# Kernel optimization log

Hardware: AMD Instinct MI355X
Metric: run time of the kernel (lower is better)

The kernel has to match this reference:

```python
import jax, jax.numpy as jnp
import numpy as np

S = 1                      # half window
K = 2 * S + 1              # box kernel size = 3
SZ = float(K ** 3)         # kernel volume = 27
EPS = 1e-5


def _box_sum(x, s=S):
    """3D box-sum filter with replicate (edge) padding.

    Equivalent to Conv3d(1,1,kernel=2s+1,padding=s,padding_mode='replicate')
    with an all-ones kernel, computed via separable sliding sums (cumsum
    difference) along D, H, W -- O(1) work per voxel per axis.
    x: [B, 1, D, H, W]
    """
    k = 2 * s + 1
    x = jnp.pad(x, ((0, 0), (0, 0), (s, s), (s, s), (s, s)), mode='edge')
    for ax in (2, 3, 4):
        c = jnp.cumsum(x, axis=ax)
        n = c.shape[ax]
        upper = jax.lax.slice_in_dim(c, k - 1, n, axis=ax)
        zero = jnp.zeros_like(jax.lax.slice_in_dim(c, 0, 1, axis=ax))
        lower = jnp.concatenate(
            [zero, jax.lax.slice_in_dim(c, 0, n - k, axis=ax)], axis=ax)
        x = upper - lower  # sliding window sum of width k
    return x


def setup_inputs() -> dict:
    key = jax.random.key(0)
    k1, k2 = jax.random.split(key)
    shape = (2, 1, 192, 192, 192)  # [B, C=1, D, H, W]
    return {
        "im_fixed": jax.random.normal(k1, shape, dtype=jnp.float32),
        "im_moving": jax.random.normal(k2, shape, dtype=jnp.float32),
    }


def reference(im_fixed, im_moving):
    u_F = _box_sum(im_fixed) / SZ          # local mean of fixed
    u_M = _box_sum(im_moving) / SZ         # local mean of moving
    dF = im_fixed - u_F
    dM = im_moving - u_M
    cross = _box_sum(dF * dM)
    var_F = _box_sum(dF * dF)
    var_M = _box_sum(dM * dM)
    z = cross * cross / (var_F * var_M + EPS)
    return -1.0 * jnp.mean(z, axis=(1, 2, 3, 4))  # [B]
```

## Files before the change

kernel.cpp:

```cpp
#include <hip/hip_runtime.h>

#define DIM 192
#define DD  (DIM * DIM)
#define DDD (DIM * DIM * DIM)
#define INV27 (1.0f / 27.0f)
#define EPS 1e-5f

#define TY 8
#define ZC 12
#define NRS (TY + 4)
#define NPR (TY + 2)

__device__ __forceinline__ int iclamp(int v, int hi) {
    return v < 0 ? 0 : (v > hi ? hi : v);
}

__global__ __launch_bounds__(512) void lcc_fused(
    const float* __restrict__ F, const float* __restrict__ M,
    float* __restrict__ out)
{
    __shared__ float RSf[NRS][DIM];
    __shared__ float RSm[NRS][DIM];
    __shared__ float PRS[3][NPR][DIM];
    __shared__ float wred[8];

    const int tid = threadIdx.x;
    const int w   = tid >> 6;
    const int t   = tid & 63;
    const int x   = 3 * t;

    const int y0 = blockIdx.y * TY;
    const int z0 = blockIdx.x * ZC;
    const int z1 = z0 + ZC;
    const int b  = blockIdx.z;

    const float* f = F + (size_t)b * DDD;
    const float* m = M + (size_t)b * DDD;

    const int  row1a = iclamp(y0 - 2 + w, DIM - 1);
    const bool has1b = (w < NRS - 8);
    const int  row1b = iclamp(y0 + 6 + w, DIM - 1);

    const int  tA    = w + 1;
    const int  prowA = iclamp(y0 - 1 + tA, DIM - 1);
    const bool hasB  = (w == 0) || (w == 7);
    const int  tB    = (w == 0) ? 0 : NPR - 1;
    const int  prowB = iclamp(y0 - 1 + tB, DIM - 1);

    const int sAm = iclamp(prowA - 1, DIM - 1) - y0 + 2;
    const int sAc = prowA - y0 + 2;
    const int sAp = iclamp(prowA + 1, DIM - 1) - y0 + 2;
    const int sBm = iclamp(prowB - 1, DIM - 1) - y0 + 2;
    const int sBc = prowB - y0 + 2;
    const int sBp = iclamp(prowB + 1, DIM - 1) - y0 + 2;

    const int yo  = y0 + w;
    const int tOm = iclamp(yo - 1, DIM - 1) - y0 + 1;
    const int tOc = w + 1;
    const int tOp = iclamp(yo + 1, DIM - 1) - y0 + 1;

    const int zpLo = (z0 - 1 > 0) ? z0 - 1 : 0;
    const int zpHi = (z1 < DIM - 1) ? z1 : DIM - 1;
    const int zcStart = (z0 - 2 > -1) ? z0 - 2 : -1;
    const int zcEnd   = z1 + 2;

    float rAf[3][3], rAm[3][3], rBf[3][3], rBm[3][3];
    float pmv[9], pcv[9], pnv[9];
#pragma unroll
    for (int i = 0; i < 3; ++i)
#pragma unroll
        for (int j = 0; j < 3; ++j) {
            rAf[i][j] = 0.f; rAm[i][j] = 0.f; rBf[i][j] = 0.f; rBm[i][j] = 0.f;
        }
#pragma unroll
    for (int i = 0; i < 9; ++i) { pmv[i] = 0.f; pcv[i] = 0.f; pnv[i] = 0.f; }

    float accz = 0.f;

    for (int zc = zcStart; zc <= zcEnd; ++zc) {
        const bool doLoad = (zc <= zpHi + 1);
        const int zcl = iclamp(zc, DIM - 1);
        const size_t zoff = (size_t)zcl * DD;

        float fa0 = 0, fa1 = 0, fa2 = 0, ma0 = 0, ma1 = 0, ma2 = 0;
        float fb0 = 0, fb1 = 0, fb2 = 0, mb0 = 0, mb1 = 0, mb2 = 0;
        if (doLoad) {
            const float* fr = f + zoff + (size_t)row1a * DIM + x;
            const float* mr = m + zoff + (size_t)row1a * DIM + x;
            fa0 = fr[0]; fa1 = fr[1]; fa2 = fr[2];
            ma0 = mr[0]; ma1 = mr[1]; ma2 = mr[2];
            if (has1b) {
                const float* fr2 = f + zoff + (size_t)row1b * DIM + x;
                const float* mr2 = m + zoff + (size_t)row1b * DIM + x;
                fb0 = fr2[0]; fb1 = fr2[1]; fb2 = fr2[2];
                mb0 = mr2[0]; mb1 = mr2[1]; mb2 = mr2[2];
            }
        }

        {
            const int zq = zc - 2;
            if (zq >= zpLo) {
#pragma unroll
                for (int i = 0; i < 9; ++i) { pmv[i] = pcv[i]; pcv[i] = pnv[i]; }
                if (zq <= zpHi) {
#pragma unroll
                    for (int q = 0; q < 3; ++q) {
                        float3 u0 = *(const float3*)&PRS[q][tOm][x];
                        float3 u1 = *(const float3*)&PRS[q][tOc][x];
                        float3 u2 = *(const float3*)&PRS[q][tOp][x];
                        pnv[q * 3 + 0] = u0.x + u1.x + u2.x;
                        pnv[q * 3 + 1] = u0.y + u1.y + u2.y;
                        pnv[q * 3 + 2] = u0.z + u1.z + u2.z;
                    }
                }
                const int zo = zc - 3;
                if (zo >= z0 && zo < z1) {
#pragma unroll
                    for (int j = 0; j < 3; ++j) {
                        float a0 = (zo == 0) ? pcv[j]     : pmv[j];
                        float a1 = (zo == 0) ? pcv[3 + j] : pmv[3 + j];
                        float a2 = (zo == 0) ? pcv[6 + j] : pmv[6 + j];
                        float c0 = (zo == DIM - 1) ? pcv[j]     : pnv[j];
                        float c1 = (zo == DIM - 1) ? pcv[3 + j] : pnv[3 + j];
                        float c2 = (zo == DIM - 1) ? pcv[6 + j] : pnv[6 + j];
                        float cross = a0 + pcv[j]     + c0;
                        float vF    = a1 + pcv[3 + j] + c1;
                        float vM    = a2 + pcv[6 + j] + c2;
                        accz += cross * cross / (vF * vM + EPS);
                    }
                }
            }
        }

        if (doLoad) {
            {
                float aL = __shfl(fa2, t - 1); aL = (t == 0)  ? fa0 : aL;
                float aR = __shfl(fa0, t + 1); aR = (t == 63) ? fa2 : aR;
                float cL = __shfl(ma2, t - 1); cL = (t == 0)  ? ma0 : cL;
                float cR = __shfl(ma0, t + 1); cR = (t == 63) ? ma2 : cR;
                *(float3*)&RSf[w][x] = make_float3(aL + fa0 + fa1, fa0 + fa1 + fa2, fa1 + fa2 + aR);
                *(float3*)&RSm[w][x] = make_float3(cL + ma0 + ma1, ma0 + ma1 + ma2, ma1 + ma2 + cR);
            }
            if (has1b) {
                float aL = __shfl(fb2, t - 1); aL = (t == 0)  ? fb0 : aL;
                float aR = __shfl(fb0, t + 1); aR = (t == 63) ? fb2 : aR;
                float cL = __shfl(mb2, t - 1); cL = (t == 0)  ? mb0 : cL;
                float cR = __shfl(mb0, t + 1); cR = (t == 63) ? mb2 : cR;
                *(float3*)&RSf[8 + w][x] = make_float3(aL + fb0 + fb1, fb0 + fb1 + fb2, fb1 + fb2 + aR);
                *(float3*)&RSm[8 + w][x] = make_float3(cL + mb0 + mb1, mb0 + mb1 + mb2, mb1 + mb2 + cR);
            }
        }
        __syncthreads();

        const int  zp    = zc - 1;
        const bool liveP = (zp >= zpLo) && (zp <= zpHi);

        float cfA0 = 0, cfA1 = 0, cfA2 = 0, cmA0 = 0, cmA1 = 0, cmA2 = 0;
        float cfB0 = 0, cfB1 = 0, cfB2 = 0, cmB0 = 0, cmB1 = 0, cmB2 = 0;
        if (liveP) {
            const size_t poff = (size_t)zp * DD;
            const float* fv = f + poff + (size_t)prowA * DIM + x;
            const float* mv = m + poff + (size_t)prowA * DIM + x;
            cfA0 = fv[0]; cfA1 = fv[1]; cfA2 = fv[2];
            cmA0 = mv[0]; cmA1 = mv[1]; cmA2 = mv[2];
            if (hasB) {
                const float* fv2 = f + poff + (size_t)prowB * DIM + x;
                const float* mv2 = m + poff + (size_t)prowB * DIM + x;
                cfB0 = fv2[0]; cfB1 = fv2[1]; cfB2 = fv2[2];
                cmB0 = mv2[0]; cmB1 = mv2[1]; cmB2 = mv2[2];
            }
        }

        if (doLoad) {
            {
                float3 q0 = *(const float3*)&RSf[sAm][x];
                float3 q1 = *(const float3*)&RSf[sAc][x];
                float3 q2 = *(const float3*)&RSf[sAp][x];
                float3 r0 = *(const float3*)&RSm[sAm][x];
                float3 r1 = *(const float3*)&RSm[sAc][x];
                float3 r2 = *(const float3*)&RSm[sAp][x];
#pragma unroll
                for (int j = 0; j < 3; ++j) {
                    rAf[0][j] = rAf[1][j]; rAf[1][j] = rAf[2][j];
                    rAm[0][j] = rAm[1][j]; rAm[1][j] = rAm[2][j];
                }
                rAf[2][0] = q0.x + q1.x + q2.x;
                rAf[2][1] = q0.y + q1.y + q2.y;
                rAf[2][2] = q0.z + q1.z + q2.z;
                rAm[2][0] = r0.x + r1.x + r2.x;
                rAm[2][1] = r0.y + r1.y + r2.y;
                rAm[2][2] = r0.z + r1.z + r2.z;
            }
            if (hasB) {
                float3 q0 = *(const float3*)&RSf[sBm][x];
                float3 q1 = *(const float3*)&RSf[sBc][x];
                float3 q2 = *(const float3*)&RSf[sBp][x];
                float3 r0 = *(const float3*)&RSm[sBm][x];
                float3 r1 = *(const float3*)&RSm[sBc][x];
                float3 r2 = *(const float3*)&RSm[sBp][x];
#pragma unroll
                for (int j = 0; j < 3; ++j) {
                    rBf[0][j] = rBf[1][j]; rBf[1][j] = rBf[2][j];
                    rBm[0][j] = rBm[1][j]; rBm[1][j] = rBm[2][j];
                }
                rBf[2][0] = q0.x + q1.x + q2.x;
                rBf[2][1] = q0.y + q1.y + q2.y;
                rBf[2][2] = q0.z + q1.z + q2.z;
                rBm[2][0] = r0.x + r1.x + r2.x;
                rBm[2][1] = r0.y + r1.y + r2.y;
                rBm[2][2] = r0.z + r1.z + r2.z;
            }
        }

        if (liveP) {
            {
                float uf0 = (rAf[0][0] + rAf[1][0] + rAf[2][0]) * INV27;
                float uf1 = (rAf[0][1] + rAf[1][1] + rAf[2][1]) * INV27;
                float uf2 = (rAf[0][2] + rAf[1][2] + rAf[2][2]) * INV27;
                float um0 = (rAm[0][0] + rAm[1][0] + rAm[2][0]) * INV27;
                float um1 = (rAm[0][1] + rAm[1][1] + rAm[2][1]) * INV27;
                float um2 = (rAm[0][2] + rAm[1][2] + rAm[2][2]) * INV27;
                float dF0 = cfA0 - uf0, dF1 = cfA1 - uf1, dF2 = cfA2 - uf2;
                float dM0 = cmA0 - um0, dM1 = cmA1 - um1, dM2 = cmA2 - um2;
                float qc0 = dF0 * dM0, qc1 = dF1 * dM1, qc2 = dF2 * dM2;
                float qf0 = dF0 * dF0, qf1 = dF1 * dF1, qf2 = dF2 * dF2;
                float qm0 = dM0 * dM0, qm1 = dM1 * dM1, qm2 = dM2 * dM2;
                float cL = __shfl(qc2, t - 1); cL = (t == 0)  ? qc0 : cL;
                float cR = __shfl(qc0, t + 1); cR = (t == 63) ? qc2 : cR;
                float fL = __shfl(qf2, t - 1); fL = (t == 0)  ? qf0 : fL;
                float fR = __shfl(qf0, t + 1); fR = (t == 63) ? qf2 : fR;
                float mL = __shfl(qm2, t - 1); mL = (t == 0)  ? qm0 : mL;
                float mR = __shfl(qm0, t + 1); mR = (t == 63) ? qm2 : mR;
                *(float3*)&PRS[0][tA][x] = make_float3(cL + qc0 + qc1, qc0 + qc1 + qc2, qc1 + qc2 + cR);
                *(float3*)&PRS[1][tA][x] = make_float3(fL + qf0 + qf1, qf0 + qf1 + qf2, qf1 + qf2 + fR);
                *(float3*)&PRS[2][tA][x] = make_float3(mL + qm0 + qm1, qm0 + qm1 + qm2, qm1 + qm2 + mR);
            }
            if (hasB) {
                float uf0 = (rBf[0][0] + rBf[1][0] + rBf[2][0]) * INV27;
                float uf1 = (rBf[0][1] + rBf[1][1] + rBf[2][1]) * INV27;
                float uf2 = (rBf[0][2] + rBf[1][2] + rBf[2][2]) * INV27;
                float um0 = (rBm[0][0] + rBm[1][0] + rBm[2][0]) * INV27;
                float um1 = (rBm[0][1] + rBm[1][1] + rBm[2][1]) * INV27;
                float um2 = (rBm[0][2] + rBm[1][2] + rBm[2][2]) * INV27;
                float dF0 = cfB0 - uf0, dF1 = cfB1 - uf1, dF2 = cfB2 - uf2;
                float dM0 = cmB0 - um0, dM1 = cmB1 - um1, dM2 = cmB2 - um2;
                float qc0 = dF0 * dM0, qc1 = dF1 * dM1, qc2 = dF2 * dM2;
                float qf0 = dF0 * dF0, qf1 = dF1 * dF1, qf2 = dF2 * dF2;
                float qm0 = dM0 * dM0, qm1 = dM1 * dM1, qm2 = dM2 * dM2;
                float cL = __shfl(qc2, t - 1); cL = (t == 0)  ? qc0 : cL;
                float cR = __shfl(qc0, t + 1); cR = (t == 63) ? qc2 : cR;
                float fL = __shfl(qf2, t - 1); fL = (t == 0)  ? qf0 : fL;
                float fR = __shfl(qf0, t + 1); fR = (t == 63) ? qf2 : fR;
                float mL = __shfl(qm2, t - 1); mL = (t == 0)  ? qm0 : mL;
                float mR = __shfl(qm0, t + 1); mR = (t == 63) ? qm2 : mR;
                *(float3*)&PRS[0][tB][x] = make_float3(cL + qc0 + qc1, qc0 + qc1 + qc2, qc1 + qc2 + cR);
                *(float3*)&PRS[1][tB][x] = make_float3(fL + qf0 + qf1, qf0 + qf1 + qf2, qf1 + qf2 + fR);
                *(float3*)&PRS[2][tB][x] = make_float3(mL + qm0 + qm1, qm0 + qm1 + qm2, qm1 + qm2 + mR);
            }
        }
        __syncthreads();
    }

    float s = accz;
#pragma unroll
    for (int off = 32; off > 0; off >>= 1) s += __shfl_down(s, off, 64);
    if (t == 0) wred[w] = s;
    __syncthreads();
    if (tid == 0) {
        float tot = 0.f;
#pragma unroll
        for (int i = 0; i < 8; ++i) tot += wred[i];
        atomicAdd(&out[b], tot * (-1.0f / (float)DDD));
    }
}

extern "C" void kernel_launch(void* const* d_in, const int* in_sizes, int n_in,
                              void* d_out, int out_size, void* d_ws, size_t ws_size,
                              hipStream_t stream)
{
    const float* F = (const float*)d_in[0];
    const float* M = (const float*)d_in[1];
    float* out = (float*)d_out;

    hipMemsetAsync(d_out, 0, (size_t)out_size * sizeof(float), stream);

    dim3 grid(DIM / ZC, DIM / TY, 2);
    lcc_fused<<<grid, 512, 0, stream>>>(F, M, out);
}
```

Baseline: 195.8 us.

## Grow y-tile to 12 rows and rebalance per-warp row assignment

Raises the y tile from 8 to 12 rows per block, so the 4-row halo recomputation is amortised over more output rows. The per-warp row assignments are rebalanced so that every warp loads two input rows, six warps compute a second product row, and four warps handle a second output row. It also hoists the centre-voxel global loads ahead of the first barrier and adds a launch-bounds minimum-blocks hint of 4. In exchange it raises register pressure from the duplicated z-ring buffers and adds LDS use per block, which may lower occupancy or cause spills.

```diff
diff --git a/kernel.cpp b/kernel.cpp
--- a/kernel.cpp
+++ b/kernel.cpp
@@ -6,16 +6,88 @@
 #define INV27 (1.0f / 27.0f)
 #define EPS 1e-5f
 
-#define TY 8
+#define TY 12
 #define ZC 12
 #define NRS (TY + 4)
 #define NPR (TY + 2)
 
+
 __device__ __forceinline__ int iclamp(int v, int hi) {
     return v < 0 ? 0 : (v > hi ? hi : v);
 }
 
-__global__ __launch_bounds__(512) void lcc_fused(
+__device__ __forceinline__ float3 xrowsum(float v0, float v1, float v2, int t) {
+    float L = __shfl(v2, t - 1); L = (t == 0)  ? v0 : L;
+    float R = __shfl(v0, t + 1); R = (t == 63) ? v2 : R;
+    return make_float3(L + v0 + v1, v0 + v1 + v2, v1 + v2 + R);
+}
+
+__device__ __forceinline__ void ringpush(float r[3][3], const float RS[][DIM],
+                                         int sm_, int sc_, int sp_, int x) {
+    float3 q0 = *(const float3*)&RS[sm_][x];
+    float3 q1 = *(const float3*)&RS[sc_][x];
+    float3 q2 = *(const float3*)&RS[sp_][x];
+    r[0][0] = r[1][0]; r[0][1] = r[1][1]; r[0][2] = r[1][2];
+    r[1][0] = r[2][0]; r[1][1] = r[2][1]; r[1][2] = r[2][2];
+    r[2][0] = q0.x + q1.x + q2.x;
+    r[2][1] = q0.y + q1.y + q2.y;
+    r[2][2] = q0.z + q1.z + q2.z;
+}
+
+__device__ __forceinline__ void products(const float rf[3][3], const float rm[3][3],
+                                         float cf0, float cf1, float cf2,
+                                         float cm0, float cm1, float cm2,
+                                         int t, int tt, int x,
+                                         float P[3][NPR][DIM]) {
+    float uf0 = (rf[0][0] + rf[1][0] + rf[2][0]) * INV27;
+    float uf1 = (rf[0][1] + rf[1][1] + rf[2][1]) * INV27;
+    float uf2 = (rf[0][2] + rf[1][2] + rf[2][2]) * INV27;
+    float um0 = (rm[0][0] + rm[1][0] + rm[2][0]) * INV27;
+    float um1 = (rm[0][1] + rm[1][1] + rm[2][1]) * INV27;
+    float um2 = (rm[0][2] + rm[1][2] + rm[2][2]) * INV27;
+    float dF0 = cf0 - uf0, dF1 = cf1 - uf1, dF2 = cf2 - uf2;
+    float dM0 = cm0 - um0, dM1 = cm1 - um1, dM2 = cm2 - um2;
+    float3 rc = xrowsum(dF0 * dM0, dF1 * dM1, dF2 * dM2, t);
+    float3 rq = xrowsum(dF0 * dF0, dF1 * dF1, dF2 * dF2, t);
+    float3 rr = xrowsum(dM0 * dM0, dM1 * dM1, dM2 * dM2, t);
+    *(float3*)&P[0][tt][x] = rc;
+    *(float3*)&P[1][tt][x] = rq;
+    *(float3*)&P[2][tt][x] = rr;
+}
+
+__device__ __forceinline__ void prs_read(const float P[3][NPR][DIM],
+                                         int tm, int tc, int tp, int x, float pn[9]) {
+#pragma unroll
+    for (int q = 0; q < 3; ++q) {
+        float3 u0 = *(const float3*)&P[q][tm][x];
+        float3 u1 = *(const float3*)&P[q][tc][x];
+        float3 u2 = *(const float3*)&P[q][tp][x];
+        pn[q * 3 + 0] = u0.x + u1.x + u2.x;
+        pn[q * 3 + 1] = u0.y + u1.y + u2.y;
+        pn[q * 3 + 2] = u0.z + u1.z + u2.z;
+    }
+}
+
+__device__ __forceinline__ float zwindow(const float pm[9], const float pc[9],
+                                         const float pn[9], int zo) {
+    float a = 0.f;
+#pragma unroll
+    for (int j = 0; j < 3; ++j) {
+        float a0 = (zo == 0) ? pc[j]     : pm[j];
+        float a1 = (zo == 0) ? pc[3 + j] : pm[3 + j];
+        float a2 = (zo == 0) ? pc[6 + j] : pm[6 + j];
+        float c0 = (zo == DIM - 1) ? pc[j]     : pn[j];
+        float c1 = (zo == DIM - 1) ? pc[3 + j] : pn[3 + j];
+        float c2 = (zo == DIM - 1) ? pc[6 + j] : pn[6 + j];
+        float cross = a0 + pc[j]     + c0;
+        float vF    = a1 + pc[3 + j] + c1;
+        float vM    = a2 + pc[6 + j] + c2;
+        a += cross * cross / (vF * vM + EPS);
+    }
+    return a;
+}
+
+__global__ __launch_bounds__(512, 4) void lcc_fused(
     const float* __restrict__ F, const float* __restrict__ M,
     float* __restrict__ out)
 {
@@ -37,14 +109,13 @@
     const float* f = F + (size_t)b * DDD;
     const float* m = M + (size_t)b * DDD;
 
-    const int  row1a = iclamp(y0 - 2 + w, DIM - 1);
-    const bool has1b = (w < NRS - 8);
-    const int  row1b = iclamp(y0 + 6 + w, DIM - 1);
+    const int row1a = iclamp(y0 - 2 + w, DIM - 1);
+    const int row1b = iclamp(y0 + 6 + w, DIM - 1);
 
     const int  tA    = w + 1;
     const int  prowA = iclamp(y0 - 1 + tA, DIM - 1);
-    const bool hasB  = (w == 0) || (w == 7);
-    const int  tB    = (w == 0) ? 0 : NPR - 1;
+    const bool hasB  = (w < 6);
+    const int  tB    = (w < 5) ? 9 + w : 0;
     const int  prowB = iclamp(y0 - 1 + tB, DIM - 1);
 
     const int sAm = iclamp(prowA - 1, DIM - 1) - y0 + 2;
@@ -54,10 +125,15 @@
     const int sBc = prowB - y0 + 2;
     const int sBp = iclamp(prowB + 1, DIM - 1) - y0 + 2;
 
-    const int yo  = y0 + w;
-    const int tOm = iclamp(yo - 1, DIM - 1) - y0 + 1;
-    const int tOc = w + 1;
-    const int tOp = iclamp(yo + 1, DIM - 1) - y0 + 1;
+    const int  yo1  = y0 + w;
+    const int  t1m  = iclamp(yo1 - 1, DIM - 1) - y0 + 1;
+    const int  t1c  = w + 1;
+    const int  t1p  = iclamp(yo1 + 1, DIM - 1) - y0 + 1;
+    const bool has2 = (w < 4);
+    const int  yo2  = y0 + 8 + w;
+    const int  t2m  = iclamp(yo2 - 1, DIM - 1) - y0 + 1;
+    const int  t2c  = 9 + w;
+    const int  t2p  = iclamp(yo2 + 1, DIM - 1) - y0 + 1;
 
     const int zpLo = (z0 - 1 > 0) ? z0 - 1 : 0;
     const int zpHi = (z1 < DIM - 1) ? z1 : DIM - 1;
@@ -65,7 +141,7 @@
     const int zcEnd   = z1 + 2;
 
     float rAf[3][3], rAm[3][3], rBf[3][3], rBm[3][3];
-    float pmv[9], pcv[9], pnv[9];
+    float pm1[9], pc1[9], pn1[9], pm2[9], pc2[9], pn2[9];
 #pragma unroll
     for (int i = 0; i < 3; ++i)
 #pragma unroll
@@ -73,14 +149,19 @@
             rAf[i][j] = 0.f; rAm[i][j] = 0.f; rBf[i][j] = 0.f; rBm[i][j] = 0.f;
         }
 #pragma unroll
-    for (int i = 0; i < 9; ++i) { pmv[i] = 0.f; pcv[i] = 0.f; pnv[i] = 0.f; }
+    for (int i = 0; i < 9; ++i) {
+        pm1[i] = 0.f; pc1[i] = 0.f; pn1[i] = 0.f;
+        pm2[i] = 0.f; pc2[i] = 0.f; pn2[i] = 0.f;
+    }
 
     float accz = 0.f;
 
     for (int zc = zcStart; zc <= zcEnd; ++zc) {
         const bool doLoad = (zc <= zpHi + 1);
-        const int zcl = iclamp(zc, DIM - 1);
+        const int  zcl  = iclamp(zc, DIM - 1);
         const size_t zoff = (size_t)zcl * DD;
+        const int  zp    = zc - 1;
+        const bool liveP = (zp >= zpLo) && (zp <= zpHi);
 
         float fa0 = 0, fa1 = 0, fa2 = 0, ma0 = 0, ma1 = 0, ma2 = 0;
         float fb0 = 0, fb1 = 0, fb2 = 0, mb0 = 0, mb1 = 0, mb2 = 0;
@@ -89,72 +170,11 @@
             const float* mr = m + zoff + (size_t)row1a * DIM + x;
             fa0 = fr[0]; fa1 = fr[1]; fa2 = fr[2];
             ma0 = mr[0]; ma1 = mr[1]; ma2 = mr[2];
-            if (has1b) {
-                const float* fr2 = f + zoff + (size_t)row1b * DIM + x;
-                const float* mr2 = m + zoff + (size_t)row1b * DIM + x;
-                fb0 = fr2[0]; fb1 = fr2[1]; fb2 = fr2[2];
-                mb0 = mr2[0]; mb1 = mr2[1]; mb2 = mr2[2];
-            }
-        }
-
-        {
-            const int zq = zc - 2;
-            if (zq >= zpLo) {
-#pragma unroll
-                for (int i = 0; i < 9; ++i) { pmv[i] = pcv[i]; pcv[i] = pnv[i]; }
-                if (zq <= zpHi) {
-#pragma unroll
-                    for (int q = 0; q < 3; ++q) {
-                        float3 u0 = *(const float3*)&PRS[q][tOm][x];
-                        float3 u1 = *(const float3*)&PRS[q][tOc][x];
-                        float3 u2 = *(const float3*)&PRS[q][tOp][x];
-                        pnv[q * 3 + 0] = u0.x + u1.x + u2.x;
-                        pnv[q * 3 + 1] = u0.y + u1.y + u2.y;
-                        pnv[q * 3 + 2] = u0.z + u1.z + u2.z;
-                    }
-                }
-                const int zo = zc - 3;
-                if (zo >= z0 && zo < z1) {
-#pragma unroll
-                    for (int j = 0; j < 3; ++j) {
-                        float a0 = (zo == 0) ? pcv[j]     : pmv[j];
-                        float a1 = (zo == 0) ? pcv[3 + j] : pmv[3 + j];
-                        float a2 = (zo == 0) ? pcv[6 + j] : pmv[6 + j];
-                        float c0 = (zo == DIM - 1) ? pcv[j]     : pnv[j];
-                        float c1 = (zo == DIM - 1) ? pcv[3 + j] : pnv[3 + j];
-                        float c2 = (zo == DIM - 1) ? pcv[6 + j] : pnv[6 + j];
-                        float cross = a0 + pcv[j]     + c0;
-                        float vF    = a1 + pcv[3 + j] + c1;
-                        float vM    = a2 + pcv[6 + j] + c2;
-                        accz += cross * cross / (vF * vM + EPS);
-                    }
-                }
-            }
-        }
-
-        if (doLoad) {
-            {
-                float aL = __shfl(fa2, t - 1); aL = (t == 0)  ? fa0 : aL;
-                float aR = __shfl(fa0, t + 1); aR = (t == 63) ? fa2 : aR;
-                float cL = __shfl(ma2, t - 1); cL = (t == 0)  ? ma0 : cL;
-                float cR = __shfl(ma0, t + 1); cR = (t == 63) ? ma2 : cR;
-                *(float3*)&RSf[w][x] = make_float3(aL + fa0 + fa1, fa0 + fa1 + fa2, fa1 + fa2 + aR);
-                *(float3*)&RSm[w][x] = make_float3(cL + ma0 + ma1, ma0 + ma1 + ma2, ma1 + ma2 + cR);
-            }
-            if (has1b) {
-                float aL = __shfl(fb2, t - 1); aL = (t == 0)  ? fb0 : aL;
-                float aR = __shfl(fb0, t + 1); aR = (t == 63) ? fb2 : aR;
-                float cL = __shfl(mb2, t - 1); cL = (t == 0)  ? mb0 : cL;
-                float cR = __shfl(mb0, t + 1); cR = (t == 63) ? mb2 : cR;
-                *(float3*)&RSf[8 + w][x] = make_float3(aL + fb0 + fb1, fb0 + fb1 + fb2, fb1 + fb2 + aR);
-                *(float3*)&RSm[8 + w][x] = make_float3(cL + mb0 + mb1, mb0 + mb1 + mb2, mb1 + mb2 + cR);
-            }
-        }
-        __syncthreads();
-
-        const int  zp    = zc - 1;
-        const bool liveP = (zp >= zpLo) && (zp <= zpHi);
-
+            const float* fr2 = f + zoff + (size_t)row1b * DIM + x;
+            const float* mr2 = m + zoff + (size_t)row1b * DIM + x;
+            fb0 = fr2[0]; fb1 = fr2[1]; fb2 = fr2[2];
+            mb0 = mr2[0]; mb1 = mr2[1]; mb2 = mr2[2];
+        }
         float cfA0 = 0, cfA1 = 0, cfA2 = 0, cmA0 = 0, cmA1 = 0, cmA2 = 0;
         float cfB0 = 0, cfB1 = 0, cfB2 = 0, cmB0 = 0, cmB1 = 0, cmB2 = 0;
         if (liveP) {
@@ -171,92 +191,51 @@
             }
         }
 
+        {
+            const int zq = zc - 2;
+            if (zq >= zpLo) {
+#pragma unroll
+                for (int i = 0; i < 9; ++i) { pm1[i] = pc1[i]; pc1[i] = pn1[i]; }
+                if (has2) {
+#pragma unroll
+                    for (int i = 0; i < 9; ++i) { pm2[i] = pc2[i]; pc2[i] = pn2[i]; }
+                }
+                if (zq <= zpHi) {
+                    prs_read(PRS, t1m, t1c, t1p, x, pn1);
+                    if (has2) prs_read(PRS, t2m, t2c, t2p, x, pn2);
+                }
+                const int zo = zc - 3;
+                if (zo >= z0 && zo < z1) {
+                    accz += zwindow(pm1, pc1, pn1, zo);
+                    if (has2) accz += zwindow(pm2, pc2, pn2, zo);
+                }
+            }
+        }
+
         if (doLoad) {
-            {
-                float3 q0 = *(const float3*)&RSf[sAm][x];
-                float3 q1 = *(const float3*)&RSf[sAc][x];
-                float3 q2 = *(const float3*)&RSf[sAp][x];
-                float3 r0 = *(const float3*)&RSm[sAm][x];
-                float3 r1 = *(const float3*)&RSm[sAc][x];
-                float3 r2 = *(const float3*)&RSm[sAp][x];
-#pragma unroll
-                for (int j = 0; j < 3; ++j) {
-                    rAf[0][j] = rAf[1][j]; rAf[1][j] = rAf[2][j];
-                    rAm[0][j] = rAm[1][j]; rAm[1][j] = rAm[2][j];
-                }
-                rAf[2][0] = q0.x + q1.x + q2.x;
-                rAf[2][1] = q0.y + q1.y + q2.y;
-                rAf[2][2] = q0.z + q1.z + q2.z;
-                rAm[2][0] = r0.x + r1.x + r2.x;
-                rAm[2][1] = r0.y + r1.y + r2.y;
-                rAm[2][2] = r0.z + r1.z + r2.z;
+            float3 sa = xrowsum(fa0, fa1, fa2, t);
+            float3 sb = xrowsum(ma0, ma1, ma2, t);
+            *(float3*)&RSf[w][x] = sa;
+            *(float3*)&RSm[w][x] = sb;
+            float3 sc = xrowsum(fb0, fb1, fb2, t);
+            float3 sd = xrowsum(mb0, mb1, mb2, t);
+            *(float3*)&RSf[8 + w][x] = sc;
+            *(float3*)&RSm[8 + w][x] = sd;
+        }
+        __syncthreads();
+
+        if (doLoad) {
+            ringpush(rAf, RSf, sAm, sAc, sAp, x);
+            ringpush(rAm, RSm, sAm, sAc, sAp, x);
+            if (hasB) {
+                ringpush(rBf, RSf, sBm, sBc, sBp, x);
+                ringpush(rBm, RSm, sBm, sBc, sBp, x);
             }
-            if (hasB) {
-                float3 q0 = *(const float3*)&RSf[sBm][x];
-                float3 q1 = *(const float3*)&RSf[sBc][x];
-                float3 q2 = *(const float3*)&RSf[sBp][x];
-                float3 r0 = *(const float3*)&RSm[sBm][x];
-                float3 r1 = *(const float3*)&RSm[sBc][x];
-                float3 r2 = *(const float3*)&RSm[sBp][x];
-#pragma unroll
-                for (int j = 0; j < 3; ++j) {
-                    rBf[0][j] = rBf[1][j]; rBf[1][j] = rBf[2][j];
-                    rBm[0][j] = rBm[1][j]; rBm[1][j] = rBm[2][j];
-                }
-                rBf[2][0] = q0.x + q1.x + q2.x;
-                rBf[2][1] = q0.y + q1.y + q2.y;
-                rBf[2][2] = q0.z + q1.z + q2.z;
-                rBm[2][0] = r0.x + r1.x + r2.x;
-                rBm[2][1] = r0.y + r1.y + r2.y;
-                rBm[2][2] = r0.z + r1.z + r2.z;
-            }
-        }
-
+        }
         if (liveP) {
-            {
-                float uf0 = (rAf[0][0] + rAf[1][0] + rAf[2][0]) * INV27;
-                float uf1 = (rAf[0][1] + rAf[1][1] + rAf[2][1]) * INV27;
-                float uf2 = (rAf[0][2] + rAf[1][2] + rAf[2][2]) * INV27;
-                float um0 = (rAm[0][0] + rAm[1][0] + rAm[2][0]) * INV27;
-                float um1 = (rAm[0][1] + rAm[1][1] + rAm[2][1]) * INV27;
-                float um2 = (rAm[0][2] + rAm[1][2] + rAm[2][2]) * INV27;
-                float dF0 = cfA0 - uf0, dF1 = cfA1 - uf1, dF2 = cfA2 - uf2;
-                float dM0 = cmA0 - um0, dM1 = cmA1 - um1, dM2 = cmA2 - um2;
-                float qc0 = dF0 * dM0, qc1 = dF1 * dM1, qc2 = dF2 * dM2;
-                float qf0 = dF0 * dF0, qf1 = dF1 * dF1, qf2 = dF2 * dF2;
-                float qm0 = dM0 * dM0, qm1 = dM1 * dM1, qm2 = dM2 * dM2;
-                float cL = __shfl(qc2, t - 1); cL = (t == 0)  ? qc0 : cL;
-                float cR = __shfl(qc0, t + 1); cR = (t == 63) ? qc2 : cR;
-                float fL = __shfl(qf2, t - 1); fL = (t == 0)  ? qf0 : fL;
-                float fR = __shfl(qf0, t + 1); fR = (t == 63) ? qf2 : fR;
-                float mL = __shfl(qm2, t - 1); mL = (t == 0)  ? qm0 : mL;
-                float mR = __shfl(qm0, t + 1); mR = (t == 63) ? qm2 : mR;
-                *(float3*)&PRS[0][tA][x] = make_float3(cL + qc0 + qc1, qc0 + qc1 + qc2, qc1 + qc2 + cR);
-                *(float3*)&PRS[1][tA][x] = make_float3(fL + qf0 + qf1, qf0 + qf1 + qf2, qf1 + qf2 + fR);
-                *(float3*)&PRS[2][tA][x] = make_float3(mL + qm0 + qm1, qm0 + qm1 + qm2, qm1 + qm2 + mR);
-            }
-            if (hasB) {
-                float uf0 = (rBf[0][0] + rBf[1][0] + rBf[2][0]) * INV27;
-                float uf1 = (rBf[0][1] + rBf[1][1] + rBf[2][1]) * INV27;
-                float uf2 = (rBf[0][2] + rBf[1][2] + rBf[2][2]) * INV27;
-                float um0 = (rBm[0][0] + rBm[1][0] + rBm[2][0]) * INV27;
-                float um1 = (rBm[0][1] + rBm[1][1] + rBm[2][1]) * INV27;
-                float um2 = (rBm[0][2] + rBm[1][2] + rBm[2][2]) * INV27;
-                float dF0 = cfB0 - uf0, dF1 = cfB1 - uf1, dF2 = cfB2 - uf2;
-                float dM0 = cmB0 - um0, dM1 = cmB1 - um1, dM2 = cmB2 - um2;
-                float qc0 = dF0 * dM0, qc1 = dF1 * dM1, qc2 = dF2 * dM2;
-                float qf0 = dF0 * dF0, qf1 = dF1 * dF1, qf2 = dF2 * dF2;
-                float qm0 = dM0 * dM0, qm1 = dM1 * dM1, qm2 = dM2 * dM2;
-                float cL = __shfl(qc2, t - 1); cL = (t == 0)  ? qc0 : cL;
-                float cR = __shfl(qc0, t + 1); cR = (t == 63) ? qc2 : cR;
-                float fL = __shfl(qf2, t - 1); fL = (t == 0)  ? qf0 : fL;
-                float fR = __shfl(qf0, t + 1); fR = (t == 63) ? qf2 : fR;
-                float mL = __shfl(qm2, t - 1); mL = (t == 0)  ? qm0 : mL;
-                float mR = __shfl(qm0, t + 1); mR = (t == 63) ? qm2 : mR;
-                *(float3*)&PRS[0][tB][x] = make_float3(cL + qc0 + qc1, qc0 + qc1 + qc2, qc1 + qc2 + cR);
-                *(float3*)&PRS[1][tB][x] = make_float3(fL + qf0 + qf1, qf0 + qf1 + qf2, qf1 + qf2 + fR);
-                *(float3*)&PRS[2][tB][x] = make_float3(mL + qm0 + qm1, qm0 + qm1 + qm2, qm1 + qm2 + mR);
-            }
+            products(rAf, rAm, cfA0, cfA1, cfA2, cmA0, cmA1, cmA2, t, tA, x, PRS);
+            if (hasB)
+                products(rBf, rBm, cfB0, cfB1, cfB2, cmB0, cmB1, cmB2, t, tB, x, PRS);
         }
         __syncthreads();
     }
```

Result: slower. 315.5 us (+61.1%).
